# Kernel tuning notes

Measured on AMD Instinct MI355X. Metric: run time of the kernel, lower is better.

Reference implementation:

```python
import jax, jax.numpy as jnp
import numpy as np

B, S, D, H = 2, 2048, 2048, 16
DH = D // H  # 128


def _rope(x, cos, sin):
    # Faithful to the source: x is (B, H, S, Dh) (already transposed), and the
    # original apply_rotary_emb slices freqs_cis[:, :H, :] and broadcasts over
    # the S axis -> rotation angle depends on head index (source quirk).
    h = x.shape[1]
    c = cos[:, :h, :][:, :, None, :]  # (1, H, 1, Dh/2)
    s = sin[:, :h, :][:, :, None, :]
    half = x.shape[-1] // 2
    re, im = x[..., :half], x[..., half:]
    return jnp.concatenate([re * c - im * s, re * s + im * c], axis=-1)


def setup_inputs() -> dict:
    key = jax.random.key(0)
    k0, k1, k2 = jax.random.split(key, 3)
    x = jax.random.normal(k0, (B, S, D), jnp.float32)
    Wqkv = jax.random.normal(k1, (D, 3 * D), jnp.float32) / np.float32(np.sqrt(D))
    bqkv = jnp.zeros((3 * D,), jnp.float32)
    Wout = jax.random.normal(k2, (D, D), jnp.float32) / np.float32(np.sqrt(D))
    bout = jnp.zeros((D,), jnp.float32)
    # standard RoPE frequency table, stored as cos/sin (unit-modulus complex)
    inv_freq = 1.0 / (10000.0 ** (np.arange(0, DH // 2, dtype=np.float32) / (DH // 2)))
    ang = np.outer(np.arange(S, dtype=np.float32), inv_freq)  # (S, Dh/2)
    freqs_cos = jnp.asarray(np.cos(ang)[None], jnp.float32)   # (1, S, Dh/2)
    freqs_sin = jnp.asarray(np.sin(ang)[None], jnp.float32)
    mask = jnp.triu(jnp.ones((S, S), bool), 1)[None, None]    # causal, True = masked
    return {"x": x, "Wqkv": Wqkv, "bqkv": bqkv, "Wout": Wout, "bout": bout,
            "freqs_cos": freqs_cos, "freqs_sin": freqs_sin, "mask": mask}


def reference(x, Wqkv, bqkv, Wout, bout, freqs_cos, freqs_sin, mask):
    b, s, d = x.shape
    scale = DH ** (-0.5)
    qkv = x @ Wqkv + bqkv                                   # (B, S, 3D)
    q, k, v = jnp.split(qkv, 3, axis=-1)
    to_heads = lambda t: t.reshape(b, s, H, DH).transpose(0, 2, 1, 3)  # (B,H,S,Dh)
    q, k, v = to_heads(q), to_heads(k), to_heads(v)
    q = _rope(q, freqs_cos, freqs_sin)
    k = _rope(k, freqs_cos, freqs_sin)
    scores = jnp.einsum('bhqd,bhkd->bhqk', q, k) * scale
    scores = jnp.where(mask, -jnp.inf, scores)
    p = jax.nn.softmax(scores, axis=-1)                     # dropout p=0 (eval)
    out = jnp.einsum('bhqk,bhkd->bhqd', p, v)
    out = out.transpose(0, 2, 1, 3).reshape(b, s, d)
    return out @ Wout + bout
```

## Files before the change

kernel.cpp:

```cpp
#include <hip/hip_runtime.h>

#define S_ 2048
#define D_ 2048
#define H_ 16
#define DH_ 128

typedef __attribute__((ext_vector_type(8))) short short8;
typedef __attribute__((ext_vector_type(4))) float f32x4;
typedef __attribute__((ext_vector_type(16))) float f32x16;
typedef __attribute__((ext_vector_type(8))) unsigned short ushort8;
typedef __attribute__((ext_vector_type(4))) unsigned short ushort4v;

__device__ __forceinline__ unsigned short f2bf(float f) {
  unsigned int u;
  __builtin_memcpy(&u, &f, 4);
  unsigned int lsb = (u >> 16) & 1u;
  u += 0x7fffu + lsb;
  return (unsigned short)(u >> 16);
}

__device__ __forceinline__ void gload_lds16(const void* g, void* l) {
  __builtin_amdgcn_global_load_lds(
      (const __attribute__((address_space(1))) unsigned int*)g,
      (__attribute__((address_space(3))) unsigned int*)l, 16, 0, 0);
}

template <int N> __device__ __forceinline__ void vmwait() {
  if constexpr (N == 8)      asm volatile("s_waitcnt vmcnt(8)" ::: "memory");
  else if constexpr (N == 6) asm volatile("s_waitcnt vmcnt(6)" ::: "memory");
  else if constexpr (N == 4) asm volatile("s_waitcnt vmcnt(4)" ::: "memory");
  else if constexpr (N == 3) asm volatile("s_waitcnt vmcnt(3)" ::: "memory");
  else if constexpr (N == 2) asm volatile("s_waitcnt vmcnt(2)" ::: "memory");
  else                       asm volatile("s_waitcnt vmcnt(0)" ::: "memory");
}

#define FENCE_ asm volatile("" ::: "memory")
#define BAR_ { FENCE_; __builtin_amdgcn_s_barrier(); FENCE_; }

__device__ __forceinline__ void prep_w_tile(
    const float* __restrict__ W, const float* __restrict__ cosb,
    const float* __restrict__ sinb, unsigned short* __restrict__ WT,
    int Nw, int rot_limit, int kt, int nt, float (*tile)[129]) {
  const int t = threadIdx.x;
#pragma unroll
  for (int i = 0; i < 4; ++i) {
    int q = i * 256 + t;
    int kl = q >> 5, cq = q & 31;
    float4 v = *(const float4*)(W + (size_t)(kt + kl) * Nw + nt + cq * 4);
    tile[kl][cq * 4 + 0] = v.x; tile[kl][cq * 4 + 1] = v.y;
    tile[kl][cq * 4 + 2] = v.z; tile[kl][cq * 4 + 3] = v.w;
  }
  __syncthreads();
  const bool rot = nt < rot_limit;
#pragma unroll
  for (int i = 0; i < 16; ++i) {
    int f = i * 256 + t;
    int kl = f & 31, nl = f >> 5;
    int ng = nt + nl;
    float val;
    if (rot) {
      int i0 = nl & 63;
      int h = (ng & 2047) >> 7;
      float c = cosb[h * 64 + i0], sn = sinb[h * 64 + i0];
      float re = tile[kl][i0], im = tile[kl][i0 + 64];
      val = (nl < 64) ? (re * c - im * sn) : (re * sn + im * c);
    } else {
      val = tile[kl][nl];
    }
    WT[(size_t)ng * 2048 + kt + kl] = f2bf(val);
  }
}

__global__ void k_prep(const float* __restrict__ x, unsigned short* __restrict__ xb,
                       const float* __restrict__ Wqkv, const float* __restrict__ Wout,
                       const float* __restrict__ cosb, const float* __restrict__ sinb,
                       unsigned short* __restrict__ wqkvT, unsigned short* __restrict__ woutT) {
  __shared__ float tile[32][129];
  const int bid = blockIdx.x;
  if (bid < 4096) {
    int idx = bid * 256 + threadIdx.x;
    const float4* xv = (const float4*)x;
    float4 a = xv[(size_t)idx * 2];
    float4 b = xv[(size_t)idx * 2 + 1];
    ushort8 o;
    o[0] = f2bf(a.x); o[1] = f2bf(a.y); o[2] = f2bf(a.z); o[3] = f2bf(a.w);
    o[4] = f2bf(b.x); o[5] = f2bf(b.y); o[6] = f2bf(b.z); o[7] = f2bf(b.w);
    *(ushort8*)(xb + (size_t)idx * 8) = o;
  } else if (bid < 7168) {
    int b2 = bid - 4096;
    prep_w_tile(Wqkv, cosb, sinb, wqkvT, 6144, 4096,
                (b2 & 63) * 32, (b2 >> 6) * 128, tile);
  } else {
    int b3 = bid - 7168;
    prep_w_tile(Wout, cosb, sinb, woutT, 2048, 0,
                (b3 & 63) * 32, (b3 >> 6) * 128, tile);
  }
}

template <int NF, int MODE>
__global__ __launch_bounds__(512, 2) void k_ms(
    const unsigned short* __restrict__ A, const unsigned short* __restrict__ Bt,
    const float* __restrict__ bias,
    unsigned short* __restrict__ Qb, unsigned short* __restrict__ Kb,
    unsigned short* __restrict__ Vt, float* __restrict__ Co) {
  constexpr int BN = NF * 64;
  constexpr int NT = 32;
  constexpr int BBASE = 65536;
  constexpr int BSZ = BN * 128;
  __shared__ unsigned char lds[BBASE + 3 * BSZ];

  const int tid = threadIdx.x, l = tid & 63, w = tid >> 6;
  const int wm = w >> 2, wn = w & 3;
  const int bid = blockIdx.x;
  int tmi = (bid & 1) * 8 + ((bid >> 3) & 7);
  int tni;
  if constexpr (NF == 3) tni = ((bid >> 1) & 3) * 8 + (bid >> 6);
  else                   tni = ((bid >> 1) & 3) * 4 + (bid >> 6);
  const int tm = tmi * 256;
  const int tn = tni * BN;

  const int sslot = (l & 7) ^ (l >> 3);
  const unsigned short* aB = A + (size_t)(tm + (l >> 3)) * 2048 + sslot * 8;
  const unsigned short* bB = Bt + (size_t)(tn + (l >> 3)) * 2048 + sslot * 8;
  const int xg = ((l >> 4) ^ (l & 7)) << 4;
  const int afo = (wm * 128 + (l & 15)) * 128 + xg;
  const int bfo = (wn * (NF * 16) + (l & 15)) * 128 + xg;

  f32x4 acc[8][NF] = {};
  short8 af[8], bf[2 * NF];

#define SAF_(ab_, u_) {                                                         \
  _Pragma("unroll") for (int i_ = 0; i_ < 4; ++i_) {                            \
    int c_ = w + i_ * 8;                                                        \
    gload_lds16(aB + (size_t)(c_ * 8) * 2048 + (u_) * 64,                       \
                lds + (ab_) + c_ * 1024); } }
#define SBF_(bs_, u_) {                                                         \
  _Pragma("unroll") for (int i_ = 0; i_ < NF; ++i_) {                           \
    int c_ = w + i_ * 8;                                                        \
    gload_lds16(bB + (size_t)(c_ * 8) * 2048 + (u_) * 64,                       \
                lds + (bs_) + c_ * 1024); } }
#define RDA2_(ab_, mh_) {                                                       \
  _Pragma("unroll") for (int m_ = 0; m_ < 4; ++m_) {                            \
    unsigned a_ = (ab_) + afo + ((mh_) * 4 + m_) * 2048;                        \
    af[m_]     = *(const short8*)(lds + a_);                                    \
    af[4 + m_] = *(const short8*)(lds + (a_ ^ 64)); } }
#define RDB2_(bb_) {                                                            \
  _Pragma("unroll") for (int n_ = 0; n_ < NF; ++n_) {                           \
    unsigned a_ = (bb_) + bfo + n_ * 2048;                                      \
    bf[n_]      = *(const short8*)(lds + a_);                                   \
    bf[NF + n_] = *(const short8*)(lds + (a_ ^ 64)); } }
#define MMF_(mh_) { __builtin_amdgcn_s_setprio(1);                              \
  _Pragma("unroll") for (int kk_ = 0; kk_ < 2; ++kk_)                           \
  _Pragma("unroll") for (int m_ = 0; m_ < 4; ++m_)                              \
  _Pragma("unroll") for (int n_ = 0; n_ < NF; ++n_)                             \
    acc[(mh_) * 4 + m_][n_] = __builtin_amdgcn_mfma_f32_16x16x32_bf16(          \
        af[kk_ * 4 + m_], bf[kk_ * NF + n_], acc[(mh_) * 4 + m_][n_], 0, 0, 0); \
  __builtin_amdgcn_s_setprio(0); }

  SAF_(0u, 0); SBF_(BBASE, 0); SBF_(BBASE + BSZ, 1);
  vmwait<NF>(); BAR_;

  int bcur = 0, bstg = 2;
#pragma unroll 1
  for (int v = 0; v < NT; ++v) {
    const unsigned ab = (unsigned)(v & 1) * 32768u;
    const unsigned an = (unsigned)((v + 1) & 1) * 32768u;
    const unsigned bb = BBASE + (unsigned)bcur * BSZ;
    const unsigned bs = BBASE + (unsigned)bstg * BSZ;
    RDB2_(bb);
    RDA2_(ab, 0);
    if (v + 1 < NT) SAF_(an, v + 1);
    MMF_(0);
    RDA2_(ab, 1);
    if (v + 2 < NT) SBF_(bs, v + 2);
    MMF_(1);
    if (v < NT - 2) { vmwait<NF>(); } else { vmwait<0>(); }
    BAR_;
    bcur = (bcur == 2) ? 0 : bcur + 1;
    bstg = (bstg == 2) ? 0 : bstg + 1;
  }
#undef SAF_
#undef SBF_
#undef RDA2_
#undef RDB2_
#undef MMF_

  const int ln = l & 15, rb4 = (l >> 4) << 2;
#pragma unroll
  for (int m = 0; m < 8; ++m) {
    int rbase = tm + wm * 128 + m * 16 + rb4;
#pragma unroll
    for (int n = 0; n < NF; ++n) {
      int colg = tn + wn * (NF * 16) + n * 16 + ln;
      float bv = bias[colg];
      if constexpr (MODE == 0) {
        int reg = colg >> 11;
        int h = (colg & 2047) >> 7, dh = colg & 127;
        if (reg == 2) {
          int b = rbase >> 11, s = rbase & 2047;
          ushort4v o;
#pragma unroll
          for (int j = 0; j < 4; ++j) o[j] = f2bf(acc[m][n][j] + bv);
          *(ushort4v*)(Vt + ((size_t)(b * H_ + h) * DH_ + dh) * S_ + s) = o;
        } else {
#pragma unroll
          for (int j = 0; j < 4; ++j) {
            int r = rbase + j;
            int b = r >> 11, s = r & 2047;
            size_t off = ((size_t)(b * H_ + h) * S_ + s) * DH_ + dh;
            float v = acc[m][n][j] + bv;
            if (reg == 0) Qb[off] = f2bf(v * 0.08838834764831845f);
            else Kb[off] = f2bf(v);
          }
        }
      } else {
#pragma unroll
        for (int j = 0; j < 4; ++j)
          Co[(size_t)(rbase + j) * 2048 + colg] = acc[m][n][j] + bv;
      }
    }
  }
}

__global__ __launch_bounds__(512) void k_attn(
    const unsigned short* __restrict__ Qb, const unsigned short* __restrict__ Kb,
    const unsigned short* __restrict__ Vt, unsigned short* __restrict__ Ob) {
  __shared__ unsigned short kls[2][8192];
  __shared__ unsigned short vls[2][8192];
  const int t = threadIdx.x, l = t & 63, w = t >> 6;
  const int id = blockIdx.x;
  const int p = id >> 5, bh = id & 31;
  const int b = bh >> 4, h = bh & 15;
  const int lq = l & 31, lh = l >> 5;
  const unsigned short* Qp = Qb + (size_t)bh * S_ * DH_;
  const unsigned short* Kp = Kb + (size_t)bh * S_ * DH_;
  const unsigned short* Vp = Vt + (size_t)bh * DH_ * S_;

  const int tile = (w < 4) ? p : (15 - p);
  const int qbw = tile * 128 + (w & 3) * 32;
  const int qrow = qbw + lq;
  const int nkv = 32 - 2 * p;

  short8 qf[8];
#pragma unroll
  for (int c = 0; c < 8; ++c)
    qf[c] = *(const short8*)(Qp + (size_t)qrow * 128 + c * 16 + lh * 8);

  f32x16 o[4] = {};
  float m = -1e30f, lsum = 0.f;

#pragma unroll
  for (int i = 0; i < 2; ++i) {
    int cid = w + i * 8;
    int krow = cid * 4 + (l >> 4);
    int kslot = (l & 15) ^ (krow & 7);
    gload_lds16(Kp + (size_t)krow * 128 + kslot * 8, &kls[0][cid * 512]);
    int vrow = cid * 8 + (l >> 3);
    int vslot = (l & 7) ^ (vrow & 7);
    gload_lds16(Vp + (size_t)vrow * S_ + vslot * 8, &vls[0][cid * 512]);
  }
  __syncthreads();

#pragma unroll 1
  for (int kvt = 0; kvt < nkv; ++kvt) {
    const int kvb = kvt * 64;
    const int cur = kvt & 1;

    if (kvt + 1 < nkv) {
      const int kvb2 = kvb + 64;
#pragma unroll
      for (int i = 0; i < 2; ++i) {
        int cid = w + i * 8;
        int krow = cid * 4 + (l >> 4);
        int kslot = (l & 15) ^ (krow & 7);
        gload_lds16(Kp + (size_t)(kvb2 + krow) * 128 + kslot * 8,
                    &kls[cur ^ 1][cid * 512]);
        int vrow = cid * 8 + (l >> 3);
        int vslot = (l & 7) ^ (vrow & 7);
        gload_lds16(Vp + (size_t)vrow * S_ + kvb2 + vslot * 8,
                    &vls[cur ^ 1][cid * 512]);
      }
    }

    if (kvb <= qbw + 31) {
      f32x16 sc0 = {}, sc1 = {};
      __builtin_amdgcn_s_setprio(1);
#pragma unroll
      for (int c = 0; c < 8; ++c) {
        int col = (c * 32 + lh * 16) ^ ((l & 7) << 4);
        short8 kf0 = *(const short8*)((const char*)kls[cur] + lq * 256 + col);
        short8 kf1 = *(const short8*)((const char*)kls[cur] + (32 + lq) * 256 + col);
        sc0 = __builtin_amdgcn_mfma_f32_32x32x16_bf16(kf0, qf[c], sc0, 0, 0, 0);
        sc1 = __builtin_amdgcn_mfma_f32_32x32x16_bf16(kf1, qf[c], sc1, 0, 0, 0);
      }
      __builtin_amdgcn_s_setprio(0);

      float xs[2][16];
      const bool diag = (kvb + 63) > qbw;
#pragma unroll
      for (int r = 0; r < 16; ++r) { xs[0][r] = sc0[r]; xs[1][r] = sc1[r]; }
      if (diag) {
#pragma unroll
        for (int kt = 0; kt < 2; ++kt)
#pragma unroll
          for (int r = 0; r < 16; ++r) {
            int kg = kvb + kt * 32 + (r & 3) + 8 * (r >> 2) + 4 * lh;
            if (kg > qrow) xs[kt][r] = -1e30f;
          }
      }
      float xm = -1e30f;
#pragma unroll
      for (int kt = 0; kt < 2; ++kt)
#pragma unroll
        for (int r = 0; r < 16; ++r) xm = fmaxf(xm, xs[kt][r]);
      xm = fmaxf(xm, __shfl_xor(xm, 32));

      if (__any(xm > m + 8.f)) {
        float nm = fmaxf(m, xm);
        float f = __expf(m - nm);
        m = nm; lsum *= f;
        float fj[16];
#pragma unroll
        for (int r = 0; r < 16; ++r)
          fj[r] = __shfl(f, (r & 3) + 8 * (r >> 2) + 4 * lh);
#pragma unroll
        for (int dt = 0; dt < 4; ++dt)
#pragma unroll
          for (int r = 0; r < 16; ++r) o[dt][r] *= fj[r];
      }
      float s = 0.f;
#pragma unroll
      for (int kt = 0; kt < 2; ++kt)
#pragma unroll
        for (int r = 0; r < 16; ++r) {
          float pv = __expf(xs[kt][r] - m);
          xs[kt][r] = pv;
          s += pv;
        }
      s += __shfl_xor(s, 32);
      lsum += s;

      short8 pa[4];
#pragma unroll
      for (int ks = 0; ks < 4; ++ks) {
        const int kt = ks >> 1;
        const int r0 = (ks & 1) * 8;
        unsigned a0d0, a0d1, a1d0, a1d1;
        asm("v_cvt_pk_bf16_f32 %0, %1, %2"
            : "=v"(a0d0) : "v"(xs[kt][r0 + 0]), "v"(xs[kt][r0 + 1]));
        asm("v_cvt_pk_bf16_f32 %0, %1, %2"
            : "=v"(a0d1) : "v"(xs[kt][r0 + 2]), "v"(xs[kt][r0 + 3]));
        asm("v_cvt_pk_bf16_f32 %0, %1, %2"
            : "=v"(a1d0) : "v"(xs[kt][r0 + 4]), "v"(xs[kt][r0 + 5]));
        asm("v_cvt_pk_bf16_f32 %0, %1, %2"
            : "=v"(a1d1) : "v"(xs[kt][r0 + 6]), "v"(xs[kt][r0 + 7]));
        asm volatile("v_permlane32_swap_b32 %0, %1" : "+v"(a0d0), "+v"(a1d0));
        asm volatile("v_permlane32_swap_b32 %0, %1" : "+v"(a0d1), "+v"(a1d1));
        unsigned tmp[4] = {a0d0, a0d1, a1d0, a1d1};
        __builtin_memcpy(&pa[ks], tmp, 16);
      }

      __builtin_amdgcn_s_setprio(1);
#pragma unroll
      for (int dt = 0; dt < 4; ++dt) {
#pragma unroll
        for (int ks = 0; ks < 4; ++ks) {
          int vrow = dt * 32 + lq;
          short8 vf = *(const short8*)((const char*)vls[cur] + vrow * 128 +
                                       ((ks * 32 + lh * 16) ^ ((vrow & 7) << 4)));
          o[dt] = __builtin_amdgcn_mfma_f32_32x32x16_bf16(pa[ks], vf, o[dt], 0, 0, 0);
        }
      }
      __builtin_amdgcn_s_setprio(0);
    }
    __syncthreads();
  }

  float inv = 1.f / lsum;
  float invj[16];
#pragma unroll
  for (int r = 0; r < 16; ++r)
    invj[r] = __shfl(inv, (r & 3) + 8 * (r >> 2) + 4 * lh);
#pragma unroll
  for (int dt = 0; dt < 4; ++dt)
#pragma unroll
    for (int r = 0; r < 16; ++r) {
      int srow = qbw + (r & 3) + 8 * (r >> 2) + 4 * lh;
      int col = h * 128 + dt * 32 + lq;
      Ob[((size_t)(b * S_ + srow)) * D_ + col] = f2bf(o[dt][r] * invj[r]);
    }
}

extern "C" void kernel_launch(void* const* d_in, const int* in_sizes, int n_in,
                              void* d_out, int out_size, void* d_ws, size_t ws_size,
                              hipStream_t stream) {
  const float* x    = (const float*)d_in[0];
  const float* Wqkv = (const float*)d_in[1];
  const float* bqkv = (const float*)d_in[2];
  const float* Wout = (const float*)d_in[3];
  const float* bout = (const float*)d_in[4];
  const float* fcos = (const float*)d_in[5];
  const float* fsin = (const float*)d_in[6];
  float* out = (float*)d_out;

  char* ws = (char*)d_ws;
  unsigned short* xbf   = (unsigned short*)(ws);
  unsigned short* wqkvT = (unsigned short*)(ws + 16777216);
  unsigned short* woutT = (unsigned short*)(ws + 41943040);
  unsigned short* Qb    = (unsigned short*)(ws + 50331648);
  unsigned short* Kb    = Qb + 8388608;
  unsigned short* Vtb   = Kb + 8388608;
  unsigned short* Ob    = xbf;

  hipLaunchKernelGGL(k_prep, dim3(8192), dim3(256), 0, stream,
                     x, xbf, Wqkv, Wout, fcos, fsin, wqkvT, woutT);
  hipLaunchKernelGGL((k_ms<3, 0>), dim3(512), dim3(512), 0, stream,
                     xbf, wqkvT, bqkv, Qb, Kb, Vtb, (float*)nullptr);
  hipLaunchKernelGGL(k_attn, dim3(256), dim3(512), 0, stream, Qb, Kb, Vtb, Ob);
  hipLaunchKernelGGL((k_ms<2, 1>), dim3(256), dim3(512), 0, stream,
                     Ob, woutT, bout, (unsigned short*)nullptr,
                     (unsigned short*)nullptr, (unsigned short*)nullptr, out);
}
```

Measured before the change: 230.6 us.

## Triple-buffer K/V tiles in attention with partial vmcnt waits

```diff
diff --git a/kernel.cpp b/kernel.cpp
--- a/kernel.cpp
+++ b/kernel.cpp
@@ -225,8 +225,8 @@
 __global__ __launch_bounds__(512) void k_attn(
     const unsigned short* __restrict__ Qb, const unsigned short* __restrict__ Kb,
     const unsigned short* __restrict__ Vt, unsigned short* __restrict__ Ob) {
-  __shared__ unsigned short kls[2][8192];
-  __shared__ unsigned short vls[2][8192];
+  __shared__ unsigned short kls[3][8192];
+  __shared__ unsigned short vls[3][8192];
   const int t = threadIdx.x, l = t & 63, w = t >> 6;
   const int id = blockIdx.x;
   const int p = id >> 5, bh = id & 31;
@@ -249,38 +249,29 @@
   f32x16 o[4] = {};
   float m = -1e30f, lsum = 0.f;
 
-#pragma unroll
-  for (int i = 0; i < 2; ++i) {
-    int cid = w + i * 8;
-    int krow = cid * 4 + (l >> 4);
-    int kslot = (l & 15) ^ (krow & 7);
-    gload_lds16(Kp + (size_t)krow * 128 + kslot * 8, &kls[0][cid * 512]);
-    int vrow = cid * 8 + (l >> 3);
-    int vslot = (l & 7) ^ (vrow & 7);
-    gload_lds16(Vp + (size_t)vrow * S_ + vslot * 8, &vls[0][cid * 512]);
-  }
-  __syncthreads();
-
+#define STG_(buf_, kvb_) {                                                      \
+  _Pragma("unroll") for (int i_ = 0; i_ < 2; ++i_) {                            \
+    int cid_ = w + i_ * 8;                                                      \
+    int krow_ = cid_ * 4 + (l >> 4);                                            \
+    int kslot_ = (l & 15) ^ (krow_ & 7);                                        \
+    gload_lds16(Kp + (size_t)((kvb_) + krow_) * 128 + kslot_ * 8,               \
+                &kls[buf_][cid_ * 512]);                                        \
+    int vrow_ = cid_ * 8 + (l >> 3);                                            \
+    int vslot_ = (l & 7) ^ (vrow_ & 7);                                         \
+    gload_lds16(Vp + (size_t)vrow_ * S_ + (kvb_) + vslot_ * 8,                  \
+                &vls[buf_][cid_ * 512]); } }
+
+  STG_(0, 0);
+  if (1 < nkv) STG_(1, 64);
+  if (1 < nkv) { vmwait<4>(); } else { vmwait<0>(); }
+  BAR_;
+
+  int cur = 0, stg = 2;
 #pragma unroll 1
   for (int kvt = 0; kvt < nkv; ++kvt) {
     const int kvb = kvt * 64;
-    const int cur = kvt & 1;
-
-    if (kvt + 1 < nkv) {
-      const int kvb2 = kvb + 64;
-#pragma unroll
-      for (int i = 0; i < 2; ++i) {
-        int cid = w + i * 8;
-        int krow = cid * 4 + (l >> 4);
-        int kslot = (l & 15) ^ (krow & 7);
-        gload_lds16(Kp + (size_t)(kvb2 + krow) * 128 + kslot * 8,
-                    &kls[cur ^ 1][cid * 512]);
-        int vrow = cid * 8 + (l >> 3);
-        int vslot = (l & 7) ^ (vrow & 7);
-        gload_lds16(Vp + (size_t)vrow * S_ + kvb2 + vslot * 8,
-                    &vls[cur ^ 1][cid * 512]);
-      }
-    }
+
+    if (kvt + 2 < nkv) STG_(stg, kvb + 128);
 
     if (kvb <= qbw + 31) {
       f32x16 sc0 = {}, sc1 = {};
@@ -373,8 +364,13 @@
       }
       __builtin_amdgcn_s_setprio(0);
     }
-    __syncthreads();
-  }
+
+    if (kvt + 2 < nkv) { vmwait<4>(); } else { vmwait<0>(); }
+    BAR_;
+    cur = (cur == 2) ? 0 : cur + 1;
+    stg = (stg == 2) ? 0 : stg + 1;
+  }
+#undef STG_
 
   float inv = 1.f / lsum;
   float invj[16];
```

Result: no change. 229.1 us, median of 2 (-0.6%).
